# Kernel tuning notes

Hardware: AMD Instinct MI355X
Metric: run time of the kernel (lower is better)

Reference implementation:

```python
import jax, jax.numpy as jnp
import numpy as np

MARGIN = 0.3
CLST_SCALE = 0.8
SEP_SCALE = 0.08
DIV_SCALE = 0.01
CONTRASTIVE_SCALE = 0.1


def setup_inputs() -> dict:
    key = jax.random.key(0)
    k1, k2, k3 = jax.random.split(key, 3)
    B, C, P, D = 16384, 100, 10, 256
    similarities = jax.random.uniform(k1, (B, C, P), jnp.float32, -1.0, 1.0)
    labels = jax.random.randint(k2, (B,), 0, C)
    prototypes = jax.random.normal(k3, (C * P, D), jnp.float32)
    starts = jnp.arange(C) * P
    proto_indices = jnp.stack([starts, starts + P], axis=1)  # [C,2] contiguous segments
    valid_mask = jnp.ones((C * P,), dtype=bool)
    return dict(similarities=similarities, labels=labels, prototypes=prototypes,
                proto_indices=proto_indices, valid_mask=valid_mask, max_prototypes=P)


def _balanced_proto_loss(similarities, prototypes, labels, proto_indices, valid_mask):
    B, C, P = similarities.shape
    T = prototypes.shape[0]
    distances = 1.0 - similarities  # [B,C,P]
    starts = proto_indices[:, 0]
    ends = proto_indices[:, 1]
    counts = ends - starts  # protos per class [C]
    INF = jnp.asarray(jnp.inf, distances.dtype)

    # mask invalid prototype slots per class, min over prototype slots
    pvalid = jnp.arange(P)[None, :] < counts[:, None]          # [C,P]
    dmask = jnp.where(pvalid[None, :, :], distances, INF)      # [B,C,P]
    min_all = jnp.min(dmask, axis=-1)                          # [B,C]

    # ---- cluster loss: min distance to own-class prototypes, class-balanced ----
    own_min = jnp.take_along_axis(min_all, labels[:, None], axis=1)[:, 0]  # [B]
    cls_n = jax.ops.segment_sum(jnp.ones_like(own_min), labels, num_segments=C)  # [C]
    cls_sum = jax.ops.segment_sum(own_min, labels, num_segments=C)
    has = cls_n > 0
    nvalid = jnp.maximum(jnp.sum(has), 1)
    mean_c = cls_sum / jnp.maximum(cls_n, 1.0)
    w = 1.0 / jnp.sqrt(cls_n + 1e-6)
    cluster_loss = jnp.sum(jnp.where(has, w * mean_c, 0.0)) / nvalid * CLST_SCALE

    # ---- separation loss: nearest prototype among all OTHER classes ----
    own_cls = jax.nn.one_hot(labels, C, dtype=bool)            # [B,C]
    other_min = jnp.min(jnp.where(own_cls, INF, min_all), axis=-1)  # [B]
    sep_term = jax.nn.relu(MARGIN - other_min)
    sep_cls_sum = jax.ops.segment_sum(sep_term, labels, num_segments=C)
    sep_loss = jnp.sum(jnp.where(has, sep_cls_sum / jnp.maximum(cls_n, 1.0), 0.0)) / nvalid * SEP_SCALE

    # ---- diversity loss: within-class prototype pairwise similarity (off-diagonal) ----
    norm = jnp.sqrt(jnp.sum(prototypes * prototypes, axis=-1, keepdims=True))
    pn = prototypes / jnp.maximum(norm, 1e-12)                 # F.normalize, eps=1e-12
    sim = pn @ pn.T                                            # [T,T]
    proto_class = jnp.searchsorted(starts, jnp.arange(T), side='right') - 1  # [T]
    same = proto_class[:, None] == proto_class[None, :]
    offdiag = ~jnp.eye(T, dtype=bool)
    pair = same & offdiag
    rel = jax.nn.relu(sim - 0.5)
    row_sum = jnp.sum(jnp.where(pair, rel, 0.0), axis=1)       # [T]
    cls_pair_sum = jax.ops.segment_sum(row_sum, proto_class, num_segments=C)
    npairs = (counts * (counts - 1)).astype(sim.dtype)
    div_valid = counts > 1
    ndv = jnp.maximum(jnp.sum(div_valid), 1)
    div_loss = jnp.sum(jnp.where(div_valid, cls_pair_sum / jnp.maximum(npairs, 1.0), 0.0)) / ndv * DIV_SCALE

    # ---- contrastive loss: mean off-diagonal sim over valid prototypes ----
    vpair = (valid_mask[:, None] & valid_mask[None, :]) & offdiag
    n_vpair = jnp.maximum(jnp.sum(vpair), 1).astype(sim.dtype)
    contrastive_loss = jnp.sum(jnp.where(vpair, sim, 0.0)) / n_vpair * CONTRASTIVE_SCALE

    total = cluster_loss + sep_loss + div_loss + contrastive_loss
    return jnp.stack([cluster_loss, sep_loss, div_loss, contrastive_loss, total])


def reference(similarities, labels, prototypes, proto_indices, valid_mask, max_prototypes):
    return _balanced_proto_loss(similarities, prototypes, labels, proto_indices, valid_mask)
```

## Files before the change

kernel.cpp:

```cpp
#include <hip/hip_runtime.h>
#include <hip/hip_bf16.h>
#include <math.h>

#define MARGIN_C 0.3f
#define CLST_SCALE 0.8f
#define SEP_SCALE 0.08f
#define DIV_SCALE 0.01f
#define CONTRASTIVE_SCALE 0.1f

#define INFF __builtin_huge_valf()
#define NVEC 64
#define SROWS 4

extern __shared__ float fk_lds[];
__global__ __launch_bounds__(256) void front_kernel(
    const float* __restrict__ sims, const int* __restrict__ labels,
    const int* __restrict__ pidx, const float* __restrict__ protos,
    float* __restrict__ inv_norm, float* __restrict__ own_arr,
    float* __restrict__ sep_arr, float* __restrict__ cls3,
    float* __restrict__ svec, double* __restrict__ diag,
    unsigned* __restrict__ done, int B, int C, int T, int D, int P,
    int nb_norm) {
    int t = threadIdx.x;
    int bid = blockIdx.x;
    if (bid < nb_norm) {
        if (bid == 0) {
            for (int i = t; i < 3 * C; i += 256) cls3[i] = 0.0f;
            for (int i = t; i < D; i += 256) svec[i] = 0.0f;
            if (t == 0) { *diag = 0.0; *done = 0u; }
        }
        int w = (bid * 256 + t) >> 6;
        int lane = t & 63;
        if (w >= T) return;
        const float* row = protos + (size_t)w * D;
        float ss = 0.0f;
        if ((D & 3) == 0) {
            for (int k = lane * 4; k < D; k += 256) {
                float4 v = *reinterpret_cast<const float4*>(row + k);
                ss += v.x * v.x + v.y * v.y + v.z * v.z + v.w * v.w;
            }
        } else {
            for (int k = lane; k < D; k += 64) { float v = row[k]; ss += v * v; }
        }
#pragma unroll
        for (int off = 32; off > 0; off >>= 1) ss += __shfl_xor(ss, off);
        if (lane == 0) inv_norm[w] = 1.0f / fmaxf(sqrtf(ss), 1e-12f);
        return;
    }
    int rowlen = C * P;
    int stride = ((rowlen + 3) & ~3) + 8;
    int cbase = (C + 3) & ~3;
    int* cnts = (int*)fk_lds;
    float* rows = fk_lds + cbase;

    for (int c = t; c < C; c += 256) cnts[c] = pidx[2 * c + 1] - pidx[2 * c];

    int b0 = (bid - nb_norm) * SROWS;
    if ((rowlen & 3) == 0) {
        int nf4 = rowlen >> 2;
#pragma unroll
        for (int r = 0; r < SROWS; ++r) {
            int b = b0 + r;
            if (b >= B) break;
            const float4* src = reinterpret_cast<const float4*>(sims + (size_t)b * rowlen);
            float* dst = rows + r * stride;
            for (int q = t; q < nf4; q += 256)
                *reinterpret_cast<float4*>(dst + 4 * q) = src[q];
        }
    } else {
#pragma unroll
        for (int r = 0; r < SROWS; ++r) {
            int b = b0 + r;
            if (b >= B) break;
            const float* src = sims + (size_t)b * rowlen;
            float* dst = rows + r * stride;
            for (int q = t; q < rowlen; q += 256) dst[q] = src[q];
        }
    }
    __syncthreads();

    int wave = t >> 6, lane = t & 63;
    int b = b0 + wave;
    if (b >= B) return;
    int label = labels[b];
    const float* row = rows + wave * stride;
    float own = INFF, other = INFF;
    for (int cc = 0; cc < C; cc += 64) {
        int c = cc + lane;
        if (c < C) {
            int cnt = cnts[c];
            const float* cb = row + c * P;
            float m = INFF;
            if ((P & 1) == 0) {
                for (int p = 0; p < P; p += 2) {
                    float2 v = *reinterpret_cast<const float2*>(cb + p);
                    float d0 = (p < cnt) ? (1.0f - v.x) : INFF;
                    float d1 = (p + 1 < cnt) ? (1.0f - v.y) : INFF;
                    m = fminf(m, fminf(d0, d1));
                }
            } else {
                for (int p = 0; p < P; ++p) {
                    float v = cb[p];
                    m = fminf(m, (p < cnt) ? (1.0f - v) : INFF);
                }
            }
            if (c == label) own = m;
            else other = fminf(other, m);
        }
    }
#pragma unroll
    for (int off = 32; off > 0; off >>= 1) {
        own = fminf(own, __shfl_xor(own, off));
        other = fminf(other, __shfl_xor(other, off));
    }
    if (lane == 0) {
        own_arr[b] = own;
        sep_arr[b] = fmaxf(MARGIN_C - other, 0.0f);
    }
}

extern __shared__ float rk_lds[];
__global__ __launch_bounds__(256) void reduce_kernel(
    const int* __restrict__ labels, const float* __restrict__ own_arr,
    const float* __restrict__ sep_arr, const int* __restrict__ pidx,
    const int* __restrict__ vmask, const float* __restrict__ protos,
    const float* __restrict__ inv_norm,
    float* __restrict__ cls3, float* __restrict__ cls_pair,
    float* __restrict__ svec, double* __restrict__ diag,
    unsigned* __restrict__ done, float* __restrict__ out,
    int B, int C, int T, int D, int P, int nSeg, unsigned nbTot) {
    __shared__ float wsum[4];
    __shared__ double rd[4];
    __shared__ unsigned lastf;
    int t = threadIdx.x;
    int bid = blockIdx.x;

    if (bid < nSeg) {
        for (int i = t; i < 3 * C; i += 256) rk_lds[i] = 0.0f;
        __syncthreads();
        int i = bid * 256 + t;
        if (i < B) {
            int lb = labels[i];
            atomicAdd(&rk_lds[lb], own_arr[i]);
            atomicAdd(&rk_lds[C + lb], 1.0f);
            atomicAdd(&rk_lds[2 * C + lb], sep_arr[i]);
        }
        __syncthreads();
        for (int i2 = t; i2 < 3 * C; i2 += 256) {
            float v = rk_lds[i2];
            if (v != 0.0f) unsafeAtomicAdd(&cls3[i2], v);
        }
    } else if (bid < nSeg + C) {
        int c = bid - nSeg;
        int s0 = pidx[2 * c], e = pidx[2 * c + 1];
        int n = e - s0;
        if (n > P) n = P;
        if (n < 0) n = 0;
        for (int idx = t; idx < n * D; idx += 256) {
            int i = (int)((unsigned)idx / (unsigned)D);
            rk_lds[idx] = protos[(size_t)s0 * D + idx] * inv_norm[s0 + i];
        }
        __syncthreads();
        int wv = t >> 6, lane = t & 63;
        int npair = n * (n - 1) / 2;
        float tot = 0.0f;
        for (int l = wv; l < npair; l += 4) {
            int i = 0, rem = l;
            while (rem >= n - 1 - i) { rem -= n - 1 - i; ++i; }
            int j = i + 1 + rem;
            float acc = 0.0f;
            for (int q = lane * 4; q < D; q += 256) {
                float4 a = *reinterpret_cast<const float4*>(&rk_lds[i * D + q]);
                float4 b = *reinterpret_cast<const float4*>(&rk_lds[j * D + q]);
                acc += a.x * b.x + a.y * b.y + a.z * b.z + a.w * b.w;
            }
#pragma unroll
            for (int off = 32; off > 0; off >>= 1) acc += __shfl_xor(acc, off);
            tot += 2.0f * fmaxf(acc - 0.5f, 0.0f);
        }
        if (lane == 0) wsum[wv] = tot;
        __syncthreads();
        if (t == 0) cls_pair[c] = wsum[0] + wsum[1] + wsum[2] + wsum[3];
    } else {
        int vb = bid - nSeg - C;
        int rpb = (T + NVEC - 1) / NVEC;
        int r0 = vb * rpb;
        int r1 = r0 + rpb;
        if (r1 > T) r1 = T;
        double sqd = 0.0;
        for (int d = t; d < D; d += 256) {
            float sv = 0.0f, sq = 0.0f;
            for (int r = r0; r < r1; ++r) {
                if (vmask[r] != 0) {
                    float v = protos[(size_t)r * D + d] * inv_norm[r];
                    sv += v;
                    sq += v * v;
                }
            }
            if (sv != 0.0f) unsafeAtomicAdd(&svec[d], sv);
            sqd += (double)sq;
        }
#pragma unroll
        for (int off = 32; off > 0; off >>= 1) sqd += __shfl_xor(sqd, off);
        if ((t & 63) == 0) rd[t >> 6] = sqd;
        __syncthreads();
        if (t == 0) {
            double s = rd[0] + rd[1] + rd[2] + rd[3];
            if (s != 0.0) unsafeAtomicAdd(diag, s);
        }
    }

    __threadfence();
    if (t == 0) lastf = (atomicAdd(done, 1u) == nbTot - 1u) ? 1u : 0u;
    __syncthreads();
    if (!lastf || t >= 64) return;
    __threadfence();
    int lane = t;
    float cl = 0.0f, sp = 0.0f, dv = 0.0f;
    int nval = 0, ndv = 0, V = 0;
    const float* cls_sum = cls3;
    const float* cls_n = cls3 + C;
    const float* sep_sum = cls3 + 2 * C;
    for (int c = lane; c < C; c += 64) {
        float n = cls_n[c];
        if (n > 0.0f) {
            nval += 1;
            float nm = fmaxf(n, 1.0f);
            float w = 1.0f / sqrtf(n + 1e-6f);
            cl += w * (cls_sum[c] / nm);
            sp += sep_sum[c] / nm;
        }
        int cnt = pidx[2 * c + 1] - pidx[2 * c];
        if (cnt > 1) {
            ndv += 1;
            float np = (float)(cnt * (cnt - 1));
            dv += cls_pair[c] / fmaxf(np, 1.0f);
        }
    }
    for (int r = lane; r < T; r += 64) V += (vmask[r] != 0) ? 1 : 0;
    double ss2 = 0.0;
    for (int d = lane; d < D; d += 64) { double v = (double)svec[d]; ss2 += v * v; }
#pragma unroll
    for (int off = 32; off > 0; off >>= 1) {
        cl += __shfl_xor(cl, off);
        sp += __shfl_xor(sp, off);
        dv += __shfl_xor(dv, off);
        nval += __shfl_xor(nval, off);
        ndv += __shfl_xor(ndv, off);
        V += __shfl_xor(V, off);
        ss2 += __shfl_xor(ss2, off);
    }
    if (lane == 0) {
        int nv = nval > 1 ? nval : 1;
        int nd = ndv > 1 ? ndv : 1;
        float cluster = cl / (float)nv * CLST_SCALE;
        float sep = sp / (float)nv * SEP_SCALE;
        float div = dv / (float)nd * DIV_SCALE;
        double contra_sum = ss2 - *diag;
        long long nvp = (long long)V * (long long)V - (long long)V;
        if (nvp < 1) nvp = 1;
        float contrastive = (float)(contra_sum / (double)nvp) * CONTRASTIVE_SCALE;
        out[0] = cluster;
        out[1] = sep;
        out[2] = div;
        out[3] = contrastive;
        out[4] = cluster + sep + div + contrastive;
    }
}

extern "C" void kernel_launch(void* const* d_in, const int* in_sizes, int n_in,
                              void* d_out, int out_size, void* d_ws, size_t ws_size,
                              hipStream_t stream) {
    const float* sims = (const float*)d_in[0];
    const int* labels = (const int*)d_in[1];
    const float* protos = (const float*)d_in[2];
    const int* pidx = (const int*)d_in[3];
    const int* vmask = (const int*)d_in[4];
    float* out = (float*)d_out;

    int B = in_sizes[1];
    int C = in_sizes[3] / 2;
    int T = in_sizes[4];
    int D = in_sizes[2] / T;
    int P = in_sizes[0] / (B * C);

    char* ws = (char*)d_ws;
    double* diag = (double*)ws;
    unsigned* done = (unsigned*)(ws + 8);
    float* cls3 = (float*)(ws + 16);
    float* cls_pair = cls3 + 3 * C;
    float* svec = cls_pair + C;
    float* inv_norm = svec + D;
    float* own_arr = inv_norm + T;
    float* sep_arr = own_arr + B;

    int nb_norm = (int)(((long long)T * 64 + 255) / 256);
    int nb_samp = (B + SROWS - 1) / SROWS;
    int rowlen = C * P;
    int stride = ((rowlen + 3) & ~3) + 8;
    int cbase = (C + 3) & ~3;
    size_t shmA = (size_t)(cbase + SROWS * stride) * sizeof(float);
    front_kernel<<<dim3(nb_norm + nb_samp), dim3(256), shmA, stream>>>(
        sims, labels, pidx, protos, inv_norm, own_arr, sep_arr,
        cls3, svec, diag, done, B, C, T, D, P, nb_norm);

    int nSeg = (B + 255) / 256;
    unsigned nbTot = (unsigned)(nSeg + C + NVEC);
    int ldsf = 3 * C;
    if (P * D > ldsf) ldsf = P * D;
    size_t shmB = (size_t)ldsf * sizeof(float);
    reduce_kernel<<<dim3(nbTot), dim3(256), shmB, stream>>>(
        labels, own_arr, sep_arr, pidx, vmask, protos, inv_norm,
        cls3, cls_pair, svec, diag, done, out, B, C, T, D, P, nSeg, nbTot);
}
```

Before: 128.9 us.

## Move prototype norm computation into reduce kernel and enlarge front blocks

The separate prototype-norm blocks in the front kernel are removed. Inverse norms are now computed inside the reduce kernel, both in the Gram blocks and in the column-sum blocks, from prototype rows staged in LDS. This drops the inv_norm global round trip and the norm work from the front kernel. Front blocks now hold up to 16 rows with one wave per row, each wave loading its own row, and they read counts from global memory instead of LDS. The cost is redundant norm computation and extra LDS staging and syncs in the reduce kernel.

```diff
diff --git a/kernel.cpp b/kernel.cpp
--- a/kernel.cpp
+++ b/kernel.cpp
@@ -10,85 +10,47 @@
 
 #define INFF __builtin_huge_valf()
 #define NVEC 64
-#define SROWS 4
 
 extern __shared__ float fk_lds[];
-__global__ __launch_bounds__(256) void front_kernel(
+__global__ __launch_bounds__(1024) void front_kernel(
     const float* __restrict__ sims, const int* __restrict__ labels,
-    const int* __restrict__ pidx, const float* __restrict__ protos,
-    float* __restrict__ inv_norm, float* __restrict__ own_arr,
-    float* __restrict__ sep_arr, float* __restrict__ cls3,
-    float* __restrict__ svec, double* __restrict__ diag,
-    unsigned* __restrict__ done, int B, int C, int T, int D, int P,
-    int nb_norm) {
+    const int* __restrict__ pidx,
+    float* __restrict__ own_arr, float* __restrict__ sep_arr,
+    float* __restrict__ cls3, float* __restrict__ svec,
+    double* __restrict__ diag, unsigned* __restrict__ done,
+    int B, int C, int D, int P, int strideF) {
     int t = threadIdx.x;
+    int nthr = blockDim.x;
+    int wave = t >> 6, lane = t & 63;
     int bid = blockIdx.x;
-    if (bid < nb_norm) {
-        if (bid == 0) {
-            for (int i = t; i < 3 * C; i += 256) cls3[i] = 0.0f;
-            for (int i = t; i < D; i += 256) svec[i] = 0.0f;
-            if (t == 0) { *diag = 0.0; *done = 0u; }
-        }
-        int w = (bid * 256 + t) >> 6;
-        int lane = t & 63;
-        if (w >= T) return;
-        const float* row = protos + (size_t)w * D;
-        float ss = 0.0f;
-        if ((D & 3) == 0) {
-            for (int k = lane * 4; k < D; k += 256) {
-                float4 v = *reinterpret_cast<const float4*>(row + k);
-                ss += v.x * v.x + v.y * v.y + v.z * v.z + v.w * v.w;
-            }
+    if (bid == 0) {
+        for (int i = t; i < 3 * C; i += nthr) cls3[i] = 0.0f;
+        for (int i = t; i < D; i += nthr) svec[i] = 0.0f;
+        if (t == 0) { *diag = 0.0; *done = 0u; }
+    }
+    int rowlen = C * P;
+    int rows = nthr >> 6;
+    int b = bid * rows + wave;
+    float* row = fk_lds + wave * strideF;
+    if (b < B) {
+        const float* src = sims + (size_t)b * rowlen;
+        if ((rowlen & 3) == 0) {
+            int nf4 = rowlen >> 2;
+            const float4* s4 = reinterpret_cast<const float4*>(src);
+            for (int q = lane; q < nf4; q += 64)
+                *reinterpret_cast<float4*>(row + 4 * q) = s4[q];
         } else {
-            for (int k = lane; k < D; k += 64) { float v = row[k]; ss += v * v; }
-        }
-#pragma unroll
-        for (int off = 32; off > 0; off >>= 1) ss += __shfl_xor(ss, off);
-        if (lane == 0) inv_norm[w] = 1.0f / fmaxf(sqrtf(ss), 1e-12f);
-        return;
-    }
-    int rowlen = C * P;
-    int stride = ((rowlen + 3) & ~3) + 8;
-    int cbase = (C + 3) & ~3;
-    int* cnts = (int*)fk_lds;
-    float* rows = fk_lds + cbase;
-
-    for (int c = t; c < C; c += 256) cnts[c] = pidx[2 * c + 1] - pidx[2 * c];
-
-    int b0 = (bid - nb_norm) * SROWS;
-    if ((rowlen & 3) == 0) {
-        int nf4 = rowlen >> 2;
-#pragma unroll
-        for (int r = 0; r < SROWS; ++r) {
-            int b = b0 + r;
-            if (b >= B) break;
-            const float4* src = reinterpret_cast<const float4*>(sims + (size_t)b * rowlen);
-            float* dst = rows + r * stride;
-            for (int q = t; q < nf4; q += 256)
-                *reinterpret_cast<float4*>(dst + 4 * q) = src[q];
-        }
-    } else {
-#pragma unroll
-        for (int r = 0; r < SROWS; ++r) {
-            int b = b0 + r;
-            if (b >= B) break;
-            const float* src = sims + (size_t)b * rowlen;
-            float* dst = rows + r * stride;
-            for (int q = t; q < rowlen; q += 256) dst[q] = src[q];
+            for (int q = lane; q < rowlen; q += 64) row[q] = src[q];
         }
     }
     __syncthreads();
-
-    int wave = t >> 6, lane = t & 63;
-    int b = b0 + wave;
     if (b >= B) return;
     int label = labels[b];
-    const float* row = rows + wave * stride;
     float own = INFF, other = INFF;
     for (int cc = 0; cc < C; cc += 64) {
         int c = cc + lane;
         if (c < C) {
-            int cnt = cnts[c];
+            int cnt = pidx[2 * c + 1] - pidx[2 * c];
             const float* cb = row + c * P;
             float m = INFF;
             if ((P & 1) == 0) {
@@ -124,16 +86,18 @@
     const int* __restrict__ labels, const float* __restrict__ own_arr,
     const float* __restrict__ sep_arr, const int* __restrict__ pidx,
     const int* __restrict__ vmask, const float* __restrict__ protos,
-    const float* __restrict__ inv_norm,
     float* __restrict__ cls3, float* __restrict__ cls_pair,
     float* __restrict__ svec, double* __restrict__ diag,
     unsigned* __restrict__ done, float* __restrict__ out,
-    int B, int C, int T, int D, int P, int nSeg, unsigned nbTot) {
+    int B, int C, int T, int D, int P, int nSeg, int rpb, int chunk,
+    unsigned nbTot) {
     __shared__ float wsum[4];
     __shared__ double rd[4];
+    __shared__ float invn[128];
+    __shared__ int vmf[128];
     __shared__ unsigned lastf;
-    int t = threadIdx.x;
-    int bid = blockIdx.x;
+    int t = threadIdx.x, bid = blockIdx.x;
+    int wv = t >> 6, lane = t & 63;
 
     if (bid < nSeg) {
         for (int i = t; i < 3 * C; i += 256) rk_lds[i] = 0.0f;
@@ -155,13 +119,19 @@
         int s0 = pidx[2 * c], e = pidx[2 * c + 1];
         int n = e - s0;
         if (n > P) n = P;
+        if (n > 128) n = 128;
         if (n < 0) n = 0;
-        for (int idx = t; idx < n * D; idx += 256) {
-            int i = (int)((unsigned)idx / (unsigned)D);
-            rk_lds[idx] = protos[(size_t)s0 * D + idx] * inv_norm[s0 + i];
-        }
-        __syncthreads();
-        int wv = t >> 6, lane = t & 63;
+        for (int idx = t; idx < n * D; idx += 256)
+            rk_lds[idx] = protos[(size_t)s0 * D + idx];
+        __syncthreads();
+        for (int i = wv; i < n; i += 4) {
+            float ss = 0.0f;
+            for (int q = lane; q < D; q += 64) { float v = rk_lds[i * D + q]; ss += v * v; }
+#pragma unroll
+            for (int off = 32; off > 0; off >>= 1) ss += __shfl_xor(ss, off);
+            if (lane == 0) invn[i] = 1.0f / fmaxf(sqrtf(ss), 1e-12f);
+        }
+        __syncthreads();
         int npair = n * (n - 1) / 2;
         float tot = 0.0f;
         for (int l = wv; l < npair; l += 4) {
@@ -169,36 +139,57 @@
             while (rem >= n - 1 - i) { rem -= n - 1 - i; ++i; }
             int j = i + 1 + rem;
             float acc = 0.0f;
-            for (int q = lane * 4; q < D; q += 256) {
-                float4 a = *reinterpret_cast<const float4*>(&rk_lds[i * D + q]);
-                float4 b = *reinterpret_cast<const float4*>(&rk_lds[j * D + q]);
-                acc += a.x * b.x + a.y * b.y + a.z * b.z + a.w * b.w;
+            if ((D & 3) == 0) {
+                for (int q = lane * 4; q < D; q += 256) {
+                    float4 a = *reinterpret_cast<const float4*>(&rk_lds[i * D + q]);
+                    float4 b = *reinterpret_cast<const float4*>(&rk_lds[j * D + q]);
+                    acc += a.x * b.x + a.y * b.y + a.z * b.z + a.w * b.w;
+                }
+            } else {
+                for (int q = lane; q < D; q += 64) acc += rk_lds[i * D + q] * rk_lds[j * D + q];
             }
 #pragma unroll
             for (int off = 32; off > 0; off >>= 1) acc += __shfl_xor(acc, off);
-            tot += 2.0f * fmaxf(acc - 0.5f, 0.0f);
+            tot += 2.0f * fmaxf(acc * invn[i] * invn[j] - 0.5f, 0.0f);
         }
         if (lane == 0) wsum[wv] = tot;
         __syncthreads();
         if (t == 0) cls_pair[c] = wsum[0] + wsum[1] + wsum[2] + wsum[3];
     } else {
         int vb = bid - nSeg - C;
-        int rpb = (T + NVEC - 1) / NVEC;
-        int r0 = vb * rpb;
-        int r1 = r0 + rpb;
+        int r0 = vb * rpb, r1 = r0 + rpb;
         if (r1 > T) r1 = T;
         double sqd = 0.0;
-        for (int d = t; d < D; d += 256) {
-            float sv = 0.0f, sq = 0.0f;
-            for (int r = r0; r < r1; ++r) {
-                if (vmask[r] != 0) {
-                    float v = protos[(size_t)r * D + d] * inv_norm[r];
-                    sv += v;
-                    sq += v * v;
+        for (int base = r0; base < r1; base += chunk) {
+            int nr = r1 - base;
+            if (nr > chunk) nr = chunk;
+            for (int idx = t; idx < nr * D; idx += 256)
+                rk_lds[idx] = protos[(size_t)base * D + idx];
+            __syncthreads();
+            for (int r = wv; r < nr; r += 4) {
+                float ss = 0.0f;
+                for (int q = lane; q < D; q += 64) { float v = rk_lds[r * D + q]; ss += v * v; }
+#pragma unroll
+                for (int off = 32; off > 0; off >>= 1) ss += __shfl_xor(ss, off);
+                if (lane == 0) {
+                    invn[r] = 1.0f / fmaxf(sqrtf(ss), 1e-12f);
+                    vmf[r] = vmask[base + r];
                 }
             }
-            if (sv != 0.0f) unsafeAtomicAdd(&svec[d], sv);
-            sqd += (double)sq;
+            __syncthreads();
+            for (int d = t; d < D; d += 256) {
+                float sv = 0.0f, sq = 0.0f;
+                for (int r = 0; r < nr; ++r) {
+                    if (vmf[r] != 0) {
+                        float v = rk_lds[r * D + d] * invn[r];
+                        sv += v;
+                        sq += v * v;
+                    }
+                }
+                if (sv != 0.0f) unsafeAtomicAdd(&svec[d], sv);
+                sqd += (double)sq;
+            }
+            __syncthreads();
         }
 #pragma unroll
         for (int off = 32; off > 0; off >>= 1) sqd += __shfl_xor(sqd, off);
@@ -215,13 +206,13 @@
     __syncthreads();
     if (!lastf || t >= 64) return;
     __threadfence();
-    int lane = t;
+    int lane2 = t;
     float cl = 0.0f, sp = 0.0f, dv = 0.0f;
     int nval = 0, ndv = 0, V = 0;
     const float* cls_sum = cls3;
     const float* cls_n = cls3 + C;
     const float* sep_sum = cls3 + 2 * C;
-    for (int c = lane; c < C; c += 64) {
+    for (int c = lane2; c < C; c += 64) {
         float n = cls_n[c];
         if (n > 0.0f) {
             nval += 1;
@@ -237,9 +228,9 @@
             dv += cls_pair[c] / fmaxf(np, 1.0f);
         }
     }
-    for (int r = lane; r < T; r += 64) V += (vmask[r] != 0) ? 1 : 0;
+    for (int r = lane2; r < T; r += 64) V += (vmask[r] != 0) ? 1 : 0;
     double ss2 = 0.0;
-    for (int d = lane; d < D; d += 64) { double v = (double)svec[d]; ss2 += v * v; }
+    for (int d = lane2; d < D; d += 64) { double v = (double)svec[d]; ss2 += v * v; }
 #pragma unroll
     for (int off = 32; off > 0; off >>= 1) {
         cl += __shfl_xor(cl, off);
@@ -250,7 +241,7 @@
         V += __shfl_xor(V, off);
         ss2 += __shfl_xor(ss2, off);
     }
-    if (lane == 0) {
+    if (lane2 == 0) {
         int nv = nval > 1 ? nval : 1;
         int nd = ndv > 1 ? ndv : 1;
         float cluster = cl / (float)nv * CLST_SCALE;
@@ -290,26 +281,35 @@
     float* cls3 = (float*)(ws + 16);
     float* cls_pair = cls3 + 3 * C;
     float* svec = cls_pair + C;
-    float* inv_norm = svec + D;
-    float* own_arr = inv_norm + T;
+    float* own_arr = svec + D;
     float* sep_arr = own_arr + B;
 
-    int nb_norm = (int)(((long long)T * 64 + 255) / 256);
-    int nb_samp = (B + SROWS - 1) / SROWS;
     int rowlen = C * P;
-    int stride = ((rowlen + 3) & ~3) + 8;
-    int cbase = (C + 3) & ~3;
-    size_t shmA = (size_t)(cbase + SROWS * stride) * sizeof(float);
-    front_kernel<<<dim3(nb_norm + nb_samp), dim3(256), shmA, stream>>>(
-        sims, labels, pidx, protos, inv_norm, own_arr, sep_arr,
-        cls3, svec, diag, done, B, C, T, D, P, nb_norm);
+    int strideF = ((rowlen + 3) & ~3) + 8;
+    int rowsPB = 65536 / (strideF * 4);
+    if (rowsPB > 16) rowsPB = 16;
+    if (rowsPB < 1) rowsPB = 1;
+    int blkA = rowsPB * 64;
+    int nbA = (B + rowsPB - 1) / rowsPB;
+    size_t shmA = (size_t)rowsPB * strideF * sizeof(float);
+    front_kernel<<<dim3(nbA), dim3(blkA), shmA, stream>>>(
+        sims, labels, pidx, own_arr, sep_arr, cls3, svec, diag, done,
+        B, C, D, P, strideF);
 
     int nSeg = (B + 255) / 256;
+    int rpb = (T + NVEC - 1) / NVEC;
+    int chunk = 57344 / (D * 4);
+    if (chunk < 1) chunk = 1;
+    if (chunk > rpb) chunk = rpb;
+    if (chunk > 128) chunk = 128;
+    int gramRows = (P < 128) ? P : 128;
+    int ldsF = 3 * C;
+    if (gramRows * D > ldsF) ldsF = gramRows * D;
+    if (chunk * D > ldsF) ldsF = chunk * D;
+    size_t shmB = (size_t)ldsF * sizeof(float);
     unsigned nbTot = (unsigned)(nSeg + C + NVEC);
-    int ldsf = 3 * C;
-    if (P * D > ldsf) ldsf = P * D;
-    size_t shmB = (size_t)ldsf * sizeof(float);
     reduce_kernel<<<dim3(nbTot), dim3(256), shmB, stream>>>(
-        labels, own_arr, sep_arr, pidx, vmask, protos, inv_norm,
-        cls3, cls_pair, svec, diag, done, out, B, C, T, D, P, nSeg, nbTot);
+        labels, own_arr, sep_arr, pidx, vmask, protos,
+        cls3, cls_pair, svec, diag, done, out,
+        B, C, T, D, P, nSeg, rpb, chunk, nbTot);
 }
```

Measured after the change: 128.6 us. Within noise of the previous version (-0.3%).
